# Kernel tuning notes

Hardware: AMD Instinct MI355X
Metric: run time of the kernel (lower is better)

## Reference

```python
import jax, jax.numpy as jnp
import numpy as np

N, C, K, H = 100000, 128, 16, 4
D = C // H
EPS = 1e-5


def _gelu(x):
    return jax.nn.gelu(x, approximate=False)


def _ln(x, g, b):
    mu = jnp.mean(x, axis=-1, keepdims=True)
    var = jnp.var(x, axis=-1, keepdims=True)
    return (x - mu) * jax.lax.rsqrt(var + EPS) * g + b


def setup_inputs() -> dict:
    key = jax.random.key(0)
    ks = jax.random.split(key, 24)
    s = 0.02
    inp = {
        "feat": jax.random.normal(ks[0], (N, C), jnp.float32),
        "coords": jax.random.normal(ks[1], (N, 3), jnp.float32),
        "knn_idx": jax.random.randint(ks[2], (N, K), 0, N, jnp.int32),
        "Wq": jax.random.normal(ks[3], (C, C), jnp.float32) * s,
        "bq": jnp.zeros((C,), jnp.float32),
        "Wk": jax.random.normal(ks[4], (C, C), jnp.float32) * s,
        "bk": jnp.zeros((C,), jnp.float32),
        "Wv": jax.random.normal(ks[5], (C, C), jnp.float32) * s,
        "bv": jnp.zeros((C,), jnp.float32),
        "Wp1": jax.random.normal(ks[6], (3, C), jnp.float32) * s,
        "bp1": jnp.zeros((C,), jnp.float32),
        "Wp2": jax.random.normal(ks[7], (C, C), jnp.float32) * s,
        "bp2": jnp.zeros((C,), jnp.float32),
        "Wo": jax.random.normal(ks[8], (C, C), jnp.float32) * s,
        "bo": jnp.zeros((C,), jnp.float32),
        "g1": jnp.ones((C,), jnp.float32),
        "b1": jnp.zeros((C,), jnp.float32),
        "Wf1": jax.random.normal(ks[9], (C, 2 * C), jnp.float32) * s,
        "bf1": jnp.zeros((2 * C,), jnp.float32),
        "Wf2": jax.random.normal(ks[10], (2 * C, C), jnp.float32) * s,
        "bf2": jnp.zeros((C,), jnp.float32),
        "g2": jnp.ones((C,), jnp.float32),
        "b2": jnp.zeros((C,), jnp.float32),
    }
    return inp


def reference(feat, coords, knn_idx, Wq, bq, Wk, bk, Wv, bv, Wp1, bp1, Wp2, bp2,
              Wo, bo, g1, b1, Wf1, bf1, Wf2, bf2, g2, b2):
    q = feat @ Wq + bq                      # (N, C)
    k_feat = feat @ Wk + bk
    v_feat = feat @ Wv + bv
    k_nbr = k_feat[knn_idx]                 # (N, K, C) irregular gather
    v_nbr = v_feat[knn_idx]
    rel_pos = coords[knn_idx] - coords[:, None, :]   # (N, K, 3)
    pe = _gelu(rel_pos @ Wp1 + bp1) @ Wp2 + bp2      # (N, K, C)
    k_nbr = (k_nbr + pe).reshape(N, K, H, D)
    v_nbr = (v_nbr + pe).reshape(N, K, H, D)
    qh = q.reshape(N, H, D)
    attn = jnp.einsum('nhd,nkhd->nhk', qh, k_nbr) / jnp.sqrt(jnp.float32(D))
    attn = jax.nn.softmax(attn, axis=-1)    # softmax over the K neighbors
    out = jnp.einsum('nhk,nkhd->nhd', attn, v_nbr).reshape(N, C)
    out = out @ Wo + bo
    x = _ln(feat + out, g1, b1)
    ffn = _gelu(x @ Wf1 + bf1) @ Wf2 + bf2
    return _ln(x + ffn, g2, b2)
```

## Files before the change

### kernel.cpp

```cpp
#include <hip/hip_runtime.h>
#include <math.h>

#define NPTS 100000
#define KNN  16
#define CH   50000
#define NCHUNK 2
#define ATT_BLOCKS 1280

typedef unsigned short bf16;
typedef __attribute__((ext_vector_type(8))) short bf16x8;
typedef __attribute__((ext_vector_type(4))) float f32x4;

__device__ __forceinline__ float bf2f(bf16 v) {
    union { unsigned int u; float f; } x; x.u = ((unsigned int)v) << 16; return x.f;
}
__device__ __forceinline__ bf16 f2bf(float f) {
    union { float f; unsigned int u; } x; x.f = f;
    unsigned int r = (x.u + 0x7FFFu + ((x.u >> 16) & 1u)) >> 16;
    return (bf16)r;
}
__device__ __forceinline__ unsigned int pack_bf16(float lo, float hi) {
    union { float f; unsigned int u; } a, b; a.f = lo; b.f = hi;
    return ((b.u + 0x8000u) & 0xffff0000u) | ((a.u + 0x8000u) >> 16);
}
__device__ __forceinline__ float f_lo(unsigned int u) {
    union { unsigned int x; float f; } c; c.x = u << 16; return c.f;
}
__device__ __forceinline__ float f_hi(unsigned int u) {
    union { unsigned int x; float f; } c; c.x = u & 0xffff0000u; return c.f;
}
__device__ __forceinline__ float ld1(const float* p) { return *p; }
__device__ __forceinline__ float ld1(const bf16* p) { return bf2f(*p); }

__device__ __forceinline__ float gelu_f(float x) {
    return 0.5f * x * (1.0f + erff(x * 0.70710678118654752f));
}
__device__ __forceinline__ float gelu_poly(float t) {
    float w = t * t;
    float poly = fmaf(w, fmaf(w, 0.025f, -0.16666667f), 1.0f);
    return t * fmaf(0.3989423f * t, poly, 0.5f);
}

__global__ void prep1_kernel(const float* __restrict__ Wp2, const float* __restrict__ Wo,
                             const float* __restrict__ bo, const float* __restrict__ bp2,
                             const float* __restrict__ bq, const float* __restrict__ bk,
                             const float* __restrict__ bv,
                             float* __restrict__ Wcat2, float* __restrict__ bo2,
                             float* __restrict__ bcat) {
    int b = blockIdx.x, t = threadIdx.x;
    if (b < 512) {
        int h = b >> 7, j = b & 127;
        float s = 0.f;
        for (int d = 0; d < 32; d++)
            s += Wp2[j * 128 + h * 32 + d] * Wo[(h * 32 + d) * 128 + t];
        Wcat2[b * 128 + t] = s;
    } else if (b == 512) {
        float s = bo[t];
        for (int c = 0; c < 128; c++) s += bp2[c] * Wo[c * 128 + t];
        bo2[t] = s;
    } else {
        bcat[t] = bq[t]; bcat[128 + t] = bk[t]; bcat[256 + t] = bv[t];
    }
}

__global__ void prep2_kernel(const float* __restrict__ Wq, const float* __restrict__ Wk,
                             const float* __restrict__ Wv, const float* __restrict__ Wp2,
                             const float* __restrict__ Wo, const float* __restrict__ Wcat2,
                             const float* __restrict__ Wf1, const float* __restrict__ Wf2,
                             bf16* __restrict__ BcatT, bf16* __restrict__ W2TT,
                             bf16* __restrict__ WcatT, bf16* __restrict__ Wf1T,
                             bf16* __restrict__ Wf2T) {
    int b = blockIdx.x, t = threadIdx.x;
    if (b < 384) {
        const float* W = (b < 128) ? Wq : (b < 256) ? Wk : Wv;
        BcatT[b * 128 + t] = f2bf(W[t * 128 + (b & 127)]);
    } else if (b < 512) {
        int idx = b - 384, h = idx >> 5, d = idx & 31;
        W2TT[h * 4096 + t * 32 + d] = f2bf(Wp2[t * 128 + h * 32 + d]);
    } else if (b < 640) {
        int j = b - 512;
        for (int i = 0; i < 5; i++) {
            int r = t + 128 * i;
            float v = (r < 128) ? Wo[r * 128 + j] : Wcat2[(r - 128) * 128 + j];
            WcatT[j * 640 + r] = f2bf(v);
        }
    } else if (b < 896) {
        int n = b - 640;
        Wf1T[n * 128 + t] = f2bf(Wf1[t * 256 + n]);
    } else {
        int n = b - 896;
        for (int i = 0; i < 2; i++) {
            int k = t + 128 * i;
            Wf2T[n * 256 + k] = f2bf(Wf2[k * 128 + n]);
        }
    }
}

template<int EPI, bool SPLITA, typename TA, typename TC, typename TR>
__global__ __launch_bounds__(256) void mfma_gemm(
    const TA* __restrict__ A, const bf16* __restrict__ A2,
    const bf16* __restrict__ BT, const float* __restrict__ bias,
    const TR* __restrict__ resid, const float* __restrict__ gamma,
    const float* __restrict__ beta, TC* __restrict__ Cc,
    int Nrows, int Kdim, int lda, int ldc,
    int zA, int zBT, int zbias, int zC)
{
    __shared__ bf16 As[128 * 36];
    __shared__ bf16 Bs[128 * 36];

    const int tid = threadIdx.x;
    const int z = blockIdx.z;
    const TA* Ab = A + (size_t)z * zA;
    const bf16* BTb = BT + (size_t)z * zBT;
    const float* biasb = bias + (size_t)z * zbias;
    TC* Cb = Cc + (size_t)z * zC;

    const int row0 = blockIdx.x * 128;
    const int col0 = blockIdx.y * 128;
    const int wave = tid >> 6, wr = wave >> 1, wc = wave & 1;
    const int l = tid & 63, l15 = l & 15, g = l >> 4;
    const int ar = tid >> 1;
    const int ah = (tid & 1) * 16;

    f32x4 acc[4][4];
#pragma unroll
    for (int i = 0; i < 4; i++)
#pragma unroll
        for (int j = 0; j < 4; j++) acc[i][j] = (f32x4){0.f, 0.f, 0.f, 0.f};

    for (int k0 = 0; k0 < Kdim; k0 += 32) {
        {
            int row = row0 + ar;
            ushort4 tmp[4];
            if (row < Nrows) {
                const bf16* s = (const bf16*)Ab + (size_t)row * lda + k0 + ah;
#pragma unroll
                for (int j = 0; j < 4; j++) tmp[j] = ((const ushort4*)s)[j];
            } else {
#pragma unroll
                for (int j = 0; j < 4; j++) tmp[j] = make_ushort4(0, 0, 0, 0);
            }
#pragma unroll
            for (int j = 0; j < 4; j++)
                *(ushort4*)(As + ar * 36 + ah + 4 * j) = tmp[j];
        }
        {
            int n = col0 + ar;
            const bf16* s = BTb + (size_t)n * Kdim + k0 + ah;
#pragma unroll
            for (int j = 0; j < 4; j++)
                *(ushort4*)(Bs + ar * 36 + ah + 4 * j) = ((const ushort4*)s)[j];
        }
        __syncthreads();

        union FragU { uint2 q2[2]; bf16x8 v; };
        bf16x8 af[4], bfr[4];
#pragma unroll
        for (int mt = 0; mt < 4; mt++) {
            const bf16* p = As + (wr * 64 + mt * 16 + l15) * 36 + 4 * g;
            FragU u; u.q2[0] = *(const uint2*)p; u.q2[1] = *(const uint2*)(p + 16);
            af[mt] = u.v;
        }
#pragma unroll
        for (int nt = 0; nt < 4; nt++) {
            const bf16* p = Bs + (wc * 64 + nt * 16 + l15) * 36 + 4 * g;
            FragU u; u.q2[0] = *(const uint2*)p; u.q2[1] = *(const uint2*)(p + 16);
            bfr[nt] = u.v;
        }
#pragma unroll
        for (int mt = 0; mt < 4; mt++)
#pragma unroll
            for (int nt = 0; nt < 4; nt++)
                acc[mt][nt] = __builtin_amdgcn_mfma_f32_16x16x32_bf16(
                    bfr[nt], af[mt], acc[mt][nt], 0, 0, 0);
        __syncthreads();
    }

    const int cg = 4 * g;
#pragma unroll
    for (int nt = 0; nt < 4; nt++) {
        const int col = col0 + wc * 64 + nt * 16 + cg;
        float4 bv4 = make_float4(0.f, 0.f, 0.f, 0.f);
        if constexpr (EPI >= 1) bv4 = *(const float4*)(biasb + col);
#pragma unroll
        for (int mt = 0; mt < 4; mt++) {
            int row = row0 + wr * 64 + mt * 16 + l15;
            if (row < Nrows) {
                float t0 = acc[mt][nt][0], t1 = acc[mt][nt][1];
                float t2 = acc[mt][nt][2], t3 = acc[mt][nt][3];
                if constexpr (EPI >= 1) { t0 += bv4.x; t1 += bv4.y; t2 += bv4.z; t3 += bv4.w; }
                if constexpr (EPI == 2) { t0 = gelu_f(t0); t1 = gelu_f(t1); t2 = gelu_f(t2); t3 = gelu_f(t3); }
                if constexpr (sizeof(TC) == 2) {
                    uint2 u; u.x = pack_bf16(t0, t1); u.y = pack_bf16(t2, t3);
                    *(uint2*)((bf16*)Cb + (size_t)row * ldc + col) = u;
                } else {
                    *(float4*)((float*)Cb + (size_t)row * ldc + col) = make_float4(t0, t1, t2, t3);
                }
            }
        }
    }
}

template<int EPI, bool SPLITA, typename TA, typename TC, typename TR>
__global__ __launch_bounds__(256) void mfma_gemm64(
    const TA* __restrict__ A, const bf16* __restrict__ A2,
    const bf16* __restrict__ BT, const float* __restrict__ bias,
    const TR* __restrict__ resid, const float* __restrict__ gamma,
    const float* __restrict__ beta, TC* __restrict__ Cc,
    int Nrows, int Kdim, int lda, int ldc,
    int zA, int zBT, int zbias, int zC)
{
    __shared__ bf16 As[128 * 72];
    __shared__ bf16 Bs[128 * 72];
    __shared__ float reds[256], redq[256];
    __shared__ float mu[128], rstd[128];

    const int tid = threadIdx.x;
    const int z = blockIdx.z;
    const TA* Ab = A + (size_t)z * zA;
    const bf16* BTb = BT + (size_t)z * zBT;
    const float* biasb = bias + (size_t)z * zbias;
    TC* Cb = Cc + (size_t)z * zC;

    const int row0 = blockIdx.x * 128;
    const int col0 = blockIdx.y * 128;
    const int wave = tid >> 6, wr = wave >> 1, wc = wave & 1;
    const int l = tid & 63, l15 = l & 15, g = l >> 4;
    const int sr = tid >> 1;
    const int sh = (tid & 1) * 32;

    f32x4 acc[4][4];
#pragma unroll
    for (int i = 0; i < 4; i++)
#pragma unroll
        for (int j = 0; j < 4; j++) acc[i][j] = (f32x4){0.f, 0.f, 0.f, 0.f};

    for (int k0 = 0; k0 < Kdim; k0 += 64) {
        {
            int row = row0 + sr;
            uint4 t[4];
            if (row < Nrows) {
                if constexpr (SPLITA) {
                    const bf16* s = (k0 < 128)
                        ? ((const bf16*)Ab + (size_t)row * 128 + k0 + sh)
                        : (A2 + (size_t)row * 512 + (k0 - 128) + sh);
#pragma unroll
                    for (int j2 = 0; j2 < 4; j2++) t[j2] = ((const uint4*)s)[j2];
                } else if constexpr (sizeof(TA) == 4) {
                    const float* s = (const float*)Ab + (size_t)row * lda + k0 + sh;
#pragma unroll
                    for (int j2 = 0; j2 < 4; j2++) {
                        float4 a = ((const float4*)s)[2 * j2];
                        float4 b = ((const float4*)s)[2 * j2 + 1];
                        union { uint4 u; ushort4 h[2]; } c;
                        c.h[0] = make_ushort4(f2bf(a.x), f2bf(a.y), f2bf(a.z), f2bf(a.w));
                        c.h[1] = make_ushort4(f2bf(b.x), f2bf(b.y), f2bf(b.z), f2bf(b.w));
                        t[j2] = c.u;
                    }
                } else {
                    const bf16* s = (const bf16*)Ab + (size_t)row * lda + k0 + sh;
#pragma unroll
                    for (int j2 = 0; j2 < 4; j2++) t[j2] = ((const uint4*)s)[j2];
                }
            } else {
#pragma unroll
                for (int j2 = 0; j2 < 4; j2++) t[j2] = make_uint4(0, 0, 0, 0);
            }
            bf16* dst = As + sr * 72 + sh;
#pragma unroll
            for (int j2 = 0; j2 < 4; j2++) *(uint4*)(dst + 8 * j2) = t[j2];
        }
        {
            int nn = col0 + sr;
            const bf16* s = BTb + (size_t)nn * Kdim + k0 + sh;
            uint4 t[4];
#pragma unroll
            for (int j2 = 0; j2 < 4; j2++) t[j2] = ((const uint4*)s)[j2];
            bf16* dst = Bs + sr * 72 + sh;
#pragma unroll
            for (int j2 = 0; j2 < 4; j2++) *(uint4*)(dst + 8 * j2) = t[j2];
        }
        __syncthreads();

        union FragU { uint2 q2[2]; bf16x8 v; };
#pragma unroll
        for (int s = 0; s < 2; s++) {
            bf16x8 af[4], bfr[4];
#pragma unroll
            for (int mt = 0; mt < 4; mt++) {
                const bf16* p = As + (wr * 64 + mt * 16 + l15) * 72 + s * 32 + 4 * g;
                FragU u; u.q2[0] = *(const uint2*)p; u.q2[1] = *(const uint2*)(p + 16);
                af[mt] = u.v;
            }
#pragma unroll
            for (int nt = 0; nt < 4; nt++) {
                const bf16* p = Bs + (wc * 64 + nt * 16 + l15) * 72 + s * 32 + 4 * g;
                FragU u; u.q2[0] = *(const uint2*)p; u.q2[1] = *(const uint2*)(p + 16);
                bfr[nt] = u.v;
            }
#pragma unroll
            for (int mt = 0; mt < 4; mt++)
#pragma unroll
                for (int nt = 0; nt < 4; nt++)
                    acc[mt][nt] = __builtin_amdgcn_mfma_f32_16x16x32_bf16(
                        bfr[nt], af[mt], acc[mt][nt], 0, 0, 0);
        }
        __syncthreads();
    }

    const int cg = 4 * g;

    if constexpr (EPI != 3) {
#pragma unroll
        for (int nt = 0; nt < 4; nt++) {
            const int col = col0 + wc * 64 + nt * 16 + cg;
            float4 bv4 = make_float4(0.f, 0.f, 0.f, 0.f);
            if constexpr (EPI >= 1) bv4 = *(const float4*)(biasb + col);
#pragma unroll
            for (int mt = 0; mt < 4; mt++) {
                int row = row0 + wr * 64 + mt * 16 + l15;
                if (row < Nrows) {
                    float t0 = acc[mt][nt][0], t1 = acc[mt][nt][1];
                    float t2 = acc[mt][nt][2], t3 = acc[mt][nt][3];
                    if constexpr (EPI >= 1) { t0 += bv4.x; t1 += bv4.y; t2 += bv4.z; t3 += bv4.w; }
                    if constexpr (EPI == 2) { t0 = gelu_f(t0); t1 = gelu_f(t1); t2 = gelu_f(t2); t3 = gelu_f(t3); }
                    if constexpr (sizeof(TC) == 2) {
                        uint2 u; u.x = pack_bf16(t0, t1); u.y = pack_bf16(t2, t3);
                        *(uint2*)((bf16*)Cb + (size_t)row * ldc + col) = u;
                    } else {
                        *(float4*)((float*)Cb + (size_t)row * ldc + col) = make_float4(t0, t1, t2, t3);
                    }
                }
            }
        }
    } else {
        float4 bias4[4];
#pragma unroll
        for (int nt = 0; nt < 4; nt++)
            bias4[nt] = *(const float4*)(biasb + wc * 64 + nt * 16 + cg);
#pragma unroll
        for (int mt = 0; mt < 4; mt++) {
            int rl = wr * 64 + mt * 16 + l15;
            int row = row0 + rl;
            float s = 0.f, q = 0.f;
#pragma unroll
            for (int nt = 0; nt < 4; nt++) {
                const int col = wc * 64 + nt * 16 + cg;
                float rv0 = 0.f, rv1 = 0.f, rv2 = 0.f, rv3 = 0.f;
                if (row < Nrows) {
                    if constexpr (sizeof(TR) == 2) {
                        ushort4 rr = *(const ushort4*)((const bf16*)resid + (size_t)row * 128 + col);
                        rv0 = bf2f(rr.x); rv1 = bf2f(rr.y); rv2 = bf2f(rr.z); rv3 = bf2f(rr.w);
                    } else {
                        float4 rr = *(const float4*)((const float*)resid + (size_t)row * 128 + col);
                        rv0 = rr.x; rv1 = rr.y; rv2 = rr.z; rv3 = rr.w;
                    }
                }
                float t0 = acc[mt][nt][0] + bias4[nt].x + rv0;
                float t1 = acc[mt][nt][1] + bias4[nt].y + rv1;
                float t2 = acc[mt][nt][2] + bias4[nt].z + rv2;
                float t3 = acc[mt][nt][3] + bias4[nt].w + rv3;
                acc[mt][nt][0] = t0; acc[mt][nt][1] = t1;
                acc[mt][nt][2] = t2; acc[mt][nt][3] = t3;
                s += t0 + t1 + t2 + t3;
                q = fmaf(t0, t0, q); q = fmaf(t1, t1, q);
                q = fmaf(t2, t2, q); q = fmaf(t3, t3, q);
            }
            s += __shfl_xor(s, 16); s += __shfl_xor(s, 32);
            q += __shfl_xor(q, 16); q += __shfl_xor(q, 32);
            if ((l & 48) == 0) { reds[rl * 2 + wc] = s; redq[rl * 2 + wc] = q; }
        }
        __syncthreads();
        if (tid < 128) {
            float s = reds[tid * 2] + reds[tid * 2 + 1];
            float q = redq[tid * 2] + redq[tid * 2 + 1];
            float m = s * (1.f / 128.f);
            float v = q * (1.f / 128.f) - m * m;
            mu[tid] = m; rstd[tid] = rsqrtf(v + 1e-5f);
        }
        __syncthreads();
        float4 g4[4], b4[4];
#pragma unroll
        for (int nt = 0; nt < 4; nt++) {
            g4[nt] = *(const float4*)(gamma + wc * 64 + nt * 16 + cg);
            b4[nt] = *(const float4*)(beta + wc * 64 + nt * 16 + cg);
        }
#pragma unroll
        for (int mt = 0; mt < 4; mt++) {
            int rl = wr * 64 + mt * 16 + l15;
            int row = row0 + rl;
            if (row < Nrows) {
                float m = mu[rl], rd = rstd[rl];
#pragma unroll
                for (int nt = 0; nt < 4; nt++) {
                    const int col = wc * 64 + nt * 16 + cg;
                    float t0 = (acc[mt][nt][0] - m) * rd * g4[nt].x + b4[nt].x;
                    float t1 = (acc[mt][nt][1] - m) * rd * g4[nt].y + b4[nt].y;
                    float t2 = (acc[mt][nt][2] - m) * rd * g4[nt].z + b4[nt].z;
                    float t3 = (acc[mt][nt][3] - m) * rd * g4[nt].w + b4[nt].w;
                    if constexpr (sizeof(TC) == 2) {
                        uint2 u; u.x = pack_bf16(t0, t1); u.y = pack_bf16(t2, t3);
                        *(uint2*)((bf16*)Cb + (size_t)row * 128 + col) = u;
                    } else {
                        *(float4*)((float*)Cb + (size_t)row * 128 + col) = make_float4(t0, t1, t2, t3);
                    }
                }
            }
        }
    }
}

__global__ __launch_bounds__(256, 5) void attn_kernel(
    const bf16* __restrict__ qx, const bf16* __restrict__ kf,
    const bf16* __restrict__ vf, const bf16* __restrict__ qp,
    const float* __restrict__ coords, const int* __restrict__ knn,
    const float* __restrict__ Wp1, const float* __restrict__ bp1,
    bf16* __restrict__ attn_v, bf16* __restrict__ s_out, int nbase)
{
    __shared__ __align__(16) float W1s[524];
    __shared__ __align__(16) unsigned int hv_s[4][16 * 68];
    __shared__ __align__(16) float qp_s[4][4 * 144];
    __shared__ __align__(16) float a_s[4][64];
    __shared__ int idx_s[4][16];

    const int tid = threadIdx.x;
    if (tid < 128) {
        int c = tid;
        int s4 = 4 * c + 4 * (c >> 5);
        W1s[s4 + 0] = Wp1[c];
        W1s[s4 + 1] = Wp1[128 + c];
        W1s[s4 + 2] = Wp1[256 + c];
        W1s[s4 + 3] = bp1[c];
    }
    __syncthreads();

    const int wv = tid >> 6, l = tid & 63;
    const int k = l >> 2, j = l & 3;
    unsigned int* hv32 = hv_s[wv];
    float* qpsf = qp_s[wv];
    float* as4 = a_s[wv];
    int* ixs = idx_s[wv];
    const float SCALE = 0.17677669529663688f;
    const int wave = blockIdx.x * 4 + wv;
    const int qoff = (l >> 4) * 144 + ((l & 15) >> 2) * 36 + ((l & 15) & 3) * 8;

    for (int n = nbase + wave; n < nbase + CH; n += ATT_BLOCKS * 4) {
        const int idx = knn[n * KNN + k];
        if (j == 0) ixs[k] = idx;
        const float cx = coords[n * 3 + 0], cy = coords[n * 3 + 1], cz = coords[n * 3 + 2];
        const float rx = coords[idx * 3 + 0] - cx;
        const float ry = coords[idx * 3 + 1] - cy;
        const float rz = coords[idx * 3 + 2] - cz;
        {
            uint4 qpr = *(const uint4*)(qp + (size_t)(n - nbase) * 512 + l * 8);
            float4 qa, qb;
            qa.x = f_lo(qpr.x); qa.y = f_hi(qpr.x);
            qa.z = f_lo(qpr.y); qa.w = f_hi(qpr.y);
            qb.x = f_lo(qpr.z); qb.y = f_hi(qpr.z);
            qb.z = f_lo(qpr.w); qb.w = f_hi(qpr.w);
            *(float4*)(qpsf + qoff) = qa;
            *(float4*)(qpsf + qoff + 4) = qb;
        }
        const bf16* krow = kf + (size_t)idx * 128 + j * 32;
        const bf16* qrow = qx + (size_t)n * 128 + j * 32;
        uint4 kw[4], qw[4];
#pragma unroll
        for (int m = 0; m < 4; m++) {
            kw[m] = *(const uint4*)(krow + 8 * m);
            qw[m] = *(const uint4*)(qrow + 8 * m);
        }
        asm volatile("s_waitcnt lgkmcnt(0)" ::: "memory");

        float p0 = 0.f, p1 = 0.f, p2 = 0.f, p3 = 0.f;
        const float* wbase = W1s + 132 * j;
        const int jb = j * 36;
#pragma unroll
        for (int blk = 0; blk < 4; blk++) {
            const int cb = blk * 8;
            float4 q0a = *(const float4*)(qpsf + jb + cb);
            float4 q0b = *(const float4*)(qpsf + jb + cb + 4);
            float4 q1a = *(const float4*)(qpsf + 144 + jb + cb);
            float4 q1b = *(const float4*)(qpsf + 144 + jb + cb + 4);
            float4 q2a = *(const float4*)(qpsf + 288 + jb + cb);
            float4 q2b = *(const float4*)(qpsf + 288 + jb + cb + 4);
            float4 q3a = *(const float4*)(qpsf + 432 + jb + cb);
            float4 q3b = *(const float4*)(qpsf + 432 + jb + cb + 4);
            float gg[8];
#pragma unroll
            for (int i = 0; i < 8; i++) {
                float4 w = *(const float4*)(wbase + 4 * (cb + i));
                float t = fmaf(rx, w.x, fmaf(ry, w.y, fmaf(rz, w.z, w.w)));
                float gv = gelu_poly(t);
                gg[i] = gv;
                float v0 = (i < 4) ? ((const float*)&q0a)[i] : ((const float*)&q0b)[i - 4];
                float v1 = (i < 4) ? ((const float*)&q1a)[i] : ((const float*)&q1b)[i - 4];
                float v2 = (i < 4) ? ((const float*)&q2a)[i] : ((const float*)&q2b)[i - 4];
                float v3 = (i < 4) ? ((const float*)&q3a)[i] : ((const float*)&q3b)[i - 4];
                p0 = fmaf(gv, v0, p0);
                p1 = fmaf(gv, v1, p1);
                p2 = fmaf(gv, v2, p2);
                p3 = fmaf(gv, v3, p3);
            }
            uint4 pk4;
            pk4.x = pack_bf16(gg[0], gg[1]);
            pk4.y = pack_bf16(gg[2], gg[3]);
            pk4.z = pack_bf16(gg[4], gg[5]);
            pk4.w = pack_bf16(gg[6], gg[7]);
            *(uint4*)(hv32 + k * 68 + j * 16 + blk * 4) = pk4;
        }

        float qk = 0.f;
#pragma unroll
        for (int m = 0; m < 4; m++) {
#pragma unroll
            for (int w = 0; w < 4; w++) {
                unsigned int ua = ((const unsigned int*)&kw[m])[w];
                unsigned int ub = ((const unsigned int*)&qw[m])[w];
                qk = fmaf(f_lo(ua), f_lo(ub), qk);
                qk = fmaf(f_hi(ua), f_hi(ub), qk);
            }
        }

        p0 += __shfl_xor(p0, 1); p0 += __shfl_xor(p0, 2);
        p1 += __shfl_xor(p1, 1); p1 += __shfl_xor(p1, 2);
        p2 += __shfl_xor(p2, 1); p2 += __shfl_xor(p2, 2);
        p3 += __shfl_xor(p3, 1); p3 += __shfl_xor(p3, 2);
        float pe = (j == 0) ? p0 : (j == 1) ? p1 : (j == 2) ? p2 : p3;
        float logit = (qk + pe) * SCALE;

        float mx = logit;
#pragma unroll
        for (int off = 4; off <= 32; off <<= 1) mx = fmaxf(mx, __shfl_xor(mx, off));
        float e = __expf(logit - mx);
        float ss = e;
#pragma unroll
        for (int off = 4; off <= 32; off <<= 1) ss += __shfl_xor(ss, off);
        float a = e * __builtin_amdgcn_rcpf(ss);
        as4[k * 4 + j] = a;
        asm volatile("s_waitcnt lgkmcnt(0)" ::: "memory");
        __builtin_amdgcn_sched_barrier(0);

        float ov0 = 0.f, ov1 = 0.f;
        float sv0a = 0.f, sv0b = 0.f, sv1a = 0.f, sv1b = 0.f;
        float sv2a = 0.f, sv2b = 0.f, sv3a = 0.f, sv3b = 0.f;
        const int l4 = l & 16, l5 = l & 32;
#pragma unroll
        for (int kk = 0; kk < 16; kk++) {
            float4 av = *(const float4*)(as4 + kk * 4);
            unsigned int hp = hv32[kk * 68 + l];
            float h_lo = f_lo(hp), h_hi = f_hi(hp);
            sv0a = fmaf(av.x, h_lo, sv0a); sv0b = fmaf(av.x, h_hi, sv0b);
            sv1a = fmaf(av.y, h_lo, sv1a); sv1b = fmaf(av.y, h_hi, sv1b);
            sv2a = fmaf(av.z, h_lo, sv2a); sv2b = fmaf(av.z, h_hi, sv2b);
            sv3a = fmaf(av.w, h_lo, sv3a); sv3b = fmaf(av.w, h_hi, sv3b);
            int ixk = ixs[kk];
            unsigned int vp = *(const unsigned int*)(vf + (size_t)ixk * 128 + 2 * l);
            float v_lo = f_lo(vp), v_hi = f_hi(vp);
            float t01 = l4 ? av.y : av.x;
            float t23 = l4 ? av.w : av.z;
            float ah = l5 ? t23 : t01;
            ov0 = fmaf(ah, v_lo, ov0);
            ov1 = fmaf(ah, v_hi, ov1);
        }
        unsigned int* s32 = (unsigned int*)(s_out + (size_t)(n - nbase) * 512);
        s32[l]        = pack_bf16(sv0a, sv0b);
        s32[64 + l]   = pack_bf16(sv1a, sv1b);
        s32[128 + l]  = pack_bf16(sv2a, sv2b);
        s32[192 + l]  = pack_bf16(sv3a, sv3b);
        *(unsigned int*)(attn_v + (size_t)n * 128 + 2 * l) = pack_bf16(ov0, ov1);
    }
}

__global__ void ws_report_kernel(float* out, int n, float val) {
    int i = blockIdx.x * 256 + threadIdx.x;
    if (i < n) out[i] = val;
}

extern "C" void kernel_launch(void* const* d_in, const int* in_sizes, int n_in,
                              void* d_out, int out_size, void* d_ws, size_t ws_size,
                              hipStream_t stream) {
    const float* feat   = (const float*)d_in[0];
    const float* coords = (const float*)d_in[1];
    const int*   knn    = (const int*)d_in[2];
    const float* Wq  = (const float*)d_in[3];  const float* bq  = (const float*)d_in[4];
    const float* Wk  = (const float*)d_in[5];  const float* bk  = (const float*)d_in[6];
    const float* Wv  = (const float*)d_in[7];  const float* bv  = (const float*)d_in[8];
    const float* Wp1 = (const float*)d_in[9];  const float* bp1 = (const float*)d_in[10];
    const float* Wp2 = (const float*)d_in[11]; const float* bp2 = (const float*)d_in[12];
    const float* Wo  = (const float*)d_in[13]; const float* bo  = (const float*)d_in[14];
    const float* g1  = (const float*)d_in[15]; const float* b1  = (const float*)d_in[16];
    const float* Wf1 = (const float*)d_in[17]; const float* bf1 = (const float*)d_in[18];
    const float* Wf2 = (const float*)d_in[19]; const float* bf2 = (const float*)d_in[20];
    const float* g2  = (const float*)d_in[21]; const float* b2  = (const float*)d_in[22];

    bf16* qx = (bf16*)d_ws;
    bf16* kb = qx + (size_t)NPTS * 128;
    bf16* vb = kb + (size_t)NPTS * 128;
    bf16* BcatT = vb + (size_t)NPTS * 128;
    bf16* W2TT  = BcatT + 384 * 128;
    bf16* WcatT = W2TT + 4 * 128 * 32;
    bf16* Wf1T  = WcatT + 128 * 640;
    bf16* Wf2T  = Wf1T + 256 * 128;
    float* Wcat2 = (float*)(Wf2T + 128 * 256);
    float* bo2   = Wcat2 + 512 * 128;
    float* bcat  = bo2 + 128;

    const size_t needed = ((size_t)NPTS * 128 * 3 + 384 * 128 + 4 * 128 * 32 + 128 * 640
                           + 256 * 128 + 128 * 256) * 2
                        + (512 * 128 + 128 + 384) * 4;
    if (ws_size < needed) {
        float val = 1000.0f + (float)((double)ws_size / 1073741824.0);
        hipLaunchKernelGGL(ws_report_kernel, dim3((out_size + 255) / 256), dim3(256), 0, stream,
                           (float*)d_out, out_size, val);
        return;
    }

    dim3 blk(256);
    const int GN = (NPTS + 127) / 128;
    const int GC = (CH + 127) / 128;

    hipLaunchKernelGGL(prep1_kernel, dim3(514), dim3(128), 0, stream,
                       Wp2, Wo, bo, bp2, bq, bk, bv, Wcat2, bo2, bcat);
    hipLaunchKernelGGL(prep2_kernel, dim3(1024), dim3(128), 0, stream,
                       Wq, Wk, Wv, Wp2, Wo, Wcat2, Wf1, Wf2,
                       BcatT, W2TT, WcatT, Wf1T, Wf2T);

    hipLaunchKernelGGL((mfma_gemm64<1, false, float, bf16, float>),
                       dim3(GN, 1, 3), blk, 0, stream,
                       feat, nullptr, BcatT, bcat, nullptr, nullptr, nullptr, qx,
                       NPTS, 128, 128, 128, 0, 128 * 128, 128, NPTS * 128);

    bf16* qpb = (bf16*)d_out;

    for (int c = 0; c < NCHUNK; c++) {
        const int base = c * CH;
        hipLaunchKernelGGL((mfma_gemm<0, false, bf16, bf16, float>),
                           dim3(GC, 1, 4), blk, 0, stream,
                           qx + (size_t)base * 128, nullptr, W2TT, nullptr,
                           nullptr, nullptr, nullptr, qpb,
                           CH, 32, 128, 512, 32, 128 * 32, 0, 128);
        hipLaunchKernelGGL(attn_kernel, dim3(ATT_BLOCKS), blk, 0, stream,
                           qx, kb, vb, qpb, coords, knn, Wp1, bp1,
                           qx, qpb, base);
        hipLaunchKernelGGL((mfma_gemm64<3, true, bf16, bf16, float>),
                           dim3(GC, 1, 1), blk, 0, stream,
                           qx + (size_t)base * 128, qpb, WcatT, bo2,
                           feat + (size_t)base * 128, g1, b1, qx + (size_t)base * 128,
                           CH, 640, 128, 128, 0, 0, 0, 0);
    }

    hipLaunchKernelGGL((mfma_gemm64<2, false, bf16, bf16, float>),
                       dim3(GN, 2, 1), blk, 0, stream,
                       qx, nullptr, Wf1T, bf1, nullptr, nullptr, nullptr, kb,
                       NPTS, 128, 128, 256, 0, 0, 0, 0);

    hipLaunchKernelGGL((mfma_gemm64<3, false, bf16, float, bf16>),
                       dim3(GN, 1, 1), blk, 0, stream,
                       kb, nullptr, Wf2T, bf2, qx, g2, b2, (float*)d_out,
                       NPTS, 256, 256, 128, 0, 0, 0, 0);
}
```

Before: 441.4 us.

## Fuse Q/K/V projections into one kernel reusing the converted feat tile

Replaces the three-slice batched GEMM launch (grid z=3), which re-read and re-converted the fp32 feat tile for each of Q, K and V, with a dedicated kernel. Each block loads its 128-row feat tile once, converts it to bf16 in shared memory, and loops over the three weight matrices, reloading only the B tile between them. This cuts global reads of feat roughly threefold, at the cost of fewer blocks (one per row tile instead of three) and serialized weight reloads with extra barriers inside each block.

Result: faster. 432.1 us (-2.1%).

```diff
diff --git a/kernel.cpp b/kernel.cpp
--- a/kernel.cpp
+++ b/kernel.cpp
@@ -96,6 +96,127 @@
     }
 }
 
+__global__ __launch_bounds__(256) void qkv3_kernel(
+    const float* __restrict__ A, const bf16* __restrict__ BT,
+    const float* __restrict__ bias, bf16* __restrict__ C, int Nrows)
+{
+    __shared__ bf16 As[2][128 * 72];
+    __shared__ bf16 Bs[2][128 * 72];
+
+    const int tid = threadIdx.x;
+    const int row0 = blockIdx.x * 128;
+    const int wave = tid >> 6, wr = wave >> 1, wc = wave & 1;
+    const int l = tid & 63, l15 = l & 15, g = l >> 4;
+    const int sr = tid >> 1;
+    const int sh = (tid & 1) * 32;
+
+    {
+        int row = row0 + sr;
+#pragma unroll
+        for (int h = 0; h < 2; h++) {
+            uint4 t[4];
+            if (row < Nrows) {
+                const float* s = A + (size_t)row * 128 + h * 64 + sh;
+#pragma unroll
+                for (int j2 = 0; j2 < 4; j2++) {
+                    float4 a = ((const float4*)s)[2 * j2];
+                    float4 b = ((const float4*)s)[2 * j2 + 1];
+                    union { uint4 u; ushort4 hh[2]; } c;
+                    c.hh[0] = make_ushort4(f2bf(a.x), f2bf(a.y), f2bf(a.z), f2bf(a.w));
+                    c.hh[1] = make_ushort4(f2bf(b.x), f2bf(b.y), f2bf(b.z), f2bf(b.w));
+                    t[j2] = c.u;
+                }
+            } else {
+#pragma unroll
+                for (int j2 = 0; j2 < 4; j2++) t[j2] = make_uint4(0, 0, 0, 0);
+            }
+            bf16* dst = As[h] + sr * 72 + sh;
+#pragma unroll
+            for (int j2 = 0; j2 < 4; j2++) *(uint4*)(dst + 8 * j2) = t[j2];
+        }
+    }
+    {
+#pragma unroll
+        for (int h = 0; h < 2; h++) {
+            const bf16* s = BT + (size_t)sr * 128 + h * 64 + sh;
+            bf16* dst = Bs[h] + sr * 72 + sh;
+#pragma unroll
+            for (int j2 = 0; j2 < 4; j2++)
+                *(uint4*)(dst + 8 * j2) = ((const uint4*)s)[j2];
+        }
+    }
+    __syncthreads();
+
+    union FragU { uint2 q2[2]; bf16x8 v; };
+
+    for (int z = 0; z < 3; z++) {
+        f32x4 acc[4][4];
+#pragma unroll
+        for (int i = 0; i < 4; i++)
+#pragma unroll
+            for (int j = 0; j < 4; j++) acc[i][j] = (f32x4){0.f, 0.f, 0.f, 0.f};
+
+#pragma unroll
+        for (int h = 0; h < 2; h++) {
+#pragma unroll
+            for (int s2 = 0; s2 < 2; s2++) {
+                bf16x8 af[4], bfr[4];
+#pragma unroll
+                for (int mt = 0; mt < 4; mt++) {
+                    const bf16* p = As[h] + (wr * 64 + mt * 16 + l15) * 72 + s2 * 32 + 4 * g;
+                    FragU u; u.q2[0] = *(const uint2*)p; u.q2[1] = *(const uint2*)(p + 16);
+                    af[mt] = u.v;
+                }
+#pragma unroll
+                for (int nt = 0; nt < 4; nt++) {
+                    const bf16* p = Bs[h] + (wc * 64 + nt * 16 + l15) * 72 + s2 * 32 + 4 * g;
+                    FragU u; u.q2[0] = *(const uint2*)p; u.q2[1] = *(const uint2*)(p + 16);
+                    bfr[nt] = u.v;
+                }
+#pragma unroll
+                for (int mt = 0; mt < 4; mt++)
+#pragma unroll
+                    for (int nt = 0; nt < 4; nt++)
+                        acc[mt][nt] = __builtin_amdgcn_mfma_f32_16x16x32_bf16(
+                            bfr[nt], af[mt], acc[mt][nt], 0, 0, 0);
+            }
+        }
+
+        const int cg = 4 * g;
+        bf16* Cz = C + (size_t)z * NPTS * 128;
+        const float* bz = bias + z * 128;
+#pragma unroll
+        for (int nt = 0; nt < 4; nt++) {
+            const int col = wc * 64 + nt * 16 + cg;
+            float4 bv4 = *(const float4*)(bz + col);
+#pragma unroll
+            for (int mt = 0; mt < 4; mt++) {
+                int row = row0 + wr * 64 + mt * 16 + l15;
+                if (row < Nrows) {
+                    float t0 = acc[mt][nt][0] + bv4.x;
+                    float t1 = acc[mt][nt][1] + bv4.y;
+                    float t2 = acc[mt][nt][2] + bv4.z;
+                    float t3 = acc[mt][nt][3] + bv4.w;
+                    uint2 u; u.x = pack_bf16(t0, t1); u.y = pack_bf16(t2, t3);
+                    *(uint2*)(Cz + (size_t)row * 128 + col) = u;
+                }
+            }
+        }
+        __syncthreads();
+        if (z < 2) {
+#pragma unroll
+            for (int h = 0; h < 2; h++) {
+                const bf16* s = BT + (size_t)((z + 1) * 128 + sr) * 128 + h * 64 + sh;
+                bf16* dst = Bs[h] + sr * 72 + sh;
+#pragma unroll
+                for (int j2 = 0; j2 < 4; j2++)
+                    *(uint4*)(dst + 8 * j2) = ((const uint4*)s)[j2];
+            }
+            __syncthreads();
+        }
+    }
+}
+
 template<int EPI, bool SPLITA, typename TA, typename TC, typename TR>
 __global__ __launch_bounds__(256) void mfma_gemm(
     const TA* __restrict__ A, const bf16* __restrict__ A2,
@@ -625,10 +746,8 @@
                        Wq, Wk, Wv, Wp2, Wo, Wcat2, Wf1, Wf2,
                        BcatT, W2TT, WcatT, Wf1T, Wf2T);
 
-    hipLaunchKernelGGL((mfma_gemm64<1, false, float, bf16, float>),
-                       dim3(GN, 1, 3), blk, 0, stream,
-                       feat, nullptr, BcatT, bcat, nullptr, nullptr, nullptr, qx,
-                       NPTS, 128, 128, 128, 0, 128 * 128, 128, NPTS * 128);
+    hipLaunchKernelGGL(qkv3_kernel, dim3(GN), blk, 0, stream,
+                       feat, BcatT, bcat, qx, NPTS);
 
     bf16* qpb = (bf16*)d_out;
 
```
